# Performance work log

Measured on AMD Instinct MI355X. Metric: run time of the kernel, lower is better.

Reference implementation:

```python
import jax, jax.numpy as jnp
import numpy as np
from jax import lax

B = 64          # graphs per batch
N0 = 1024       # nodes per graph (equal-sized graphs -> static topk shapes)
DEG = 16        # avg degree
E = B * N0 * DEG
D_IN, D_H, D_OUT = 100, 128, 256
RATIO, EPS = 0.5, 1e-5


def _seg_sum(v, idx, n):
    return jax.ops.segment_sum(v, idx, num_segments=n)


def _gcn(x, src, dst, w_e, W, b, n):
    h = x @ W
    deg = 1.0 + _seg_sum(w_e, dst, n)          # +1 for self-loop
    dinv = lax.rsqrt(deg)
    norm = (dinv[src] * dinv[dst] * w_e)[:, None]
    return _seg_sum(h[src] * norm, dst, n) + h / deg[:, None] + b


def _graphnorm(x, w, bias, ms, nb, k):
    # PyG GraphNorm: per-graph mean/var with learnable mean_scale
    xg = x.reshape(nb, k, -1)
    mean = xg.mean(1, keepdims=True)
    sub = xg - ms * mean
    var = (sub * sub).mean(1, keepdims=True)
    return (w * sub * lax.rsqrt(var + EPS) + bias).reshape(nb * k, -1)


def _topk(x, src, dst, emask, p, nb, n_per):
    # TopKPooling (min_score=None): score = tanh(x.p/||p||), keep top ceil(r*n)
    k = int(np.ceil(RATIO * n_per))
    score = jnp.tanh((x @ p) / jnp.linalg.norm(p))
    vals, idx = lax.top_k(score.reshape(nb, n_per), k)            # [nb, k]
    perm = (idx + (jnp.arange(nb) * n_per)[:, None]).reshape(-1)
    x_new = x[perm] * vals.reshape(-1)[:, None]
    mapping = jnp.full((nb * n_per,), -1, jnp.int32).at[perm].set(
        jnp.arange(nb * k, dtype=jnp.int32))
    ns, nd = mapping[src], mapping[dst]
    valid = emask & (ns >= 0) & (nd >= 0)   # filter_adj as a persistent mask
    return x_new, jnp.where(valid, ns, 0), jnp.where(valid, nd, 0), valid, k


def _forward(x, edge_index, W1, b1, W2, b2, W3, b3,
             gn1_w, gn1_b, gn1_ms, gn2_w, gn2_b, gn2_ms,
             gn3_w, gn3_b, gn3_ms, p1, p2, p3):
    src, dst = edge_index[0], edge_index[1]
    emask = jnp.ones(src.shape, bool)
    Ws, bs = (W1, W2, W3), (b1, b2, b3)
    gw = (gn1_w, gn2_w, gn3_w)
    gb = (gn1_b, gn2_b, gn3_b)
    gm = (gn1_ms, gn2_ms, gn3_ms)
    ps = (p1, p2, p3)
    n_per = N0
    for i in range(3):
        n = B * n_per
        x = _gcn(x, src, dst, emask.astype(x.dtype), Ws[i], bs[i], n)
        x = _graphnorm(x, gw[i], gb[i], gm[i], B, n_per)
        x = jax.nn.relu(x)              # dropout: identity in eval mode
        x, src, dst, emask, n_per = _topk(x, src, dst, emask, ps[i], B, n_per)
    xg = x.reshape(B, n_per, D_OUT)
    # global mean/max pool then concat -> [B, 2*D_OUT]
    return jnp.concatenate([xg.mean(1), xg.max(1)], axis=1)


def setup_inputs():
    key = jax.random.key(0)
    ks = jax.random.split(key, 20)
    x = jax.random.normal(ks[0], (B * N0, D_IN), jnp.float32)
    # random edges within each graph, then offset by graph base index
    e = jax.random.randint(ks[1], (2, B, N0 * DEG), 0, N0, jnp.int32)
    edge_index = (e + (jnp.arange(B, dtype=jnp.int32) * N0)[None, :, None]).reshape(2, -1)
    batch = jnp.repeat(jnp.arange(B, dtype=jnp.int32), N0)
    inp = dict(x=x, edge_index=edge_index, batch=batch)
    dims = [(D_IN, D_H), (D_H, D_H), (D_H, D_OUT)]
    for i, (di, do) in enumerate(dims, 1):
        inp[f"W{i}"] = jax.random.normal(ks[1 + i], (di, do), jnp.float32) / np.sqrt(di)
        inp[f"b{i}"] = jnp.zeros((do,), jnp.float32)
        inp[f"gn{i}_w"] = jnp.ones((do,), jnp.float32)
        inp[f"gn{i}_b"] = jnp.zeros((do,), jnp.float32)
        inp[f"gn{i}_ms"] = jnp.ones((do,), jnp.float32)
        inp[f"p{i}"] = jax.random.normal(ks[10 + i], (do,), jnp.float32)
    return inp


def reference(x, edge_index, batch, W1, b1, W2, b2, W3, b3,
              gn1_w, gn1_b, gn1_ms, gn2_w, gn2_b, gn2_ms,
              gn3_w, gn3_b, gn3_ms, p1, p2, p3):
    del batch  # equal-sized graphs: grouping is encoded by constants B, N0
    return _forward(x, edge_index, W1, b1, W2, b2, W3, b3,
                    gn1_w, gn1_b, gn1_ms, gn2_w, gn2_b, gn2_ms,
                    gn3_w, gn3_b, gn3_ms, p1, p2, p3)
```

## Files before the change

### kernel.cpp

```cpp
#include <hip/hip_runtime.h>

#define GN_EPS 1e-5f

constexpr int NB   = 64;
constexpr int EPG  = 16384;
constexpr int ETOT = NB * EPG;
constexpr int NTOT = 64 * 1024;

__global__ void cmap_init_kernel(int* __restrict__ cmap) {
    int i = blockIdx.x * blockDim.x + threadIdx.x;
    if (i < NTOT) cmap[i] = i;
}

template <int NPG>
__global__ __launch_bounds__(1024) void csr_build_kernel(
        const int* __restrict__ ei, const int* __restrict__ cmap,
        int* __restrict__ cnt, int* __restrict__ offs, float* __restrict__ dinv,
        int2* __restrict__ csr_pack) {
    __shared__ int   lcnt[NPG];
    __shared__ float sdv[NPG];
    __shared__ int   wsum[16];
    constexpr int NW = NPG / 64;
    const int g = blockIdx.x;
    const int t = threadIdx.x;
    const int ebase = g * EPG;
    constexpr int EPT = EPG / 1024;

    for (int i = t; i < NPG; i += 1024) lcnt[i] = 0;
    __syncthreads();

    int ms_[EPT], md_[EPT];
#pragma unroll
    for (int i = 0; i < EPT; i++) {
        int e = ebase + t + i * 1024;
        int s = cmap[ei[e]];
        int d = cmap[ei[ETOT + e]];
        bool ok = (s >= 0) && (d >= 0);
        ms_[i] = ok ? s : -1;
        md_[i] = ok ? (d - g * NPG) : 0;
        if (ok) atomicAdd(&lcnt[d - g * NPG], 1);
    }
    __syncthreads();

    const int lane = t & 63;
    const int wid  = t >> 6;
    int orig = (t < NPG) ? lcnt[t] : 0;
    int v = orig;
#pragma unroll
    for (int d = 1; d < 64; d <<= 1) {
        int u = __shfl_up(v, d);
        if (lane >= d) v += u;
    }
    if (lane == 63) wsum[wid] = v;
    __syncthreads();
    if (wid == 0) {
        int wv = (lane < NW) ? wsum[lane] : 0;
#pragma unroll
        for (int d = 1; d < 16; d <<= 1) {
            int u = __shfl_up(wv, d);
            if (lane >= d) wv += u;
        }
        if (lane < NW) wsum[lane] = wv;
    }
    __syncthreads();
    if (t < NPG) {
        int incl = v + ((wid > 0) ? wsum[wid - 1] : 0);
        int excl = incl - orig;
        float dv = rsqrtf(1.0f + (float)orig);
        cnt[g * NPG + t]  = orig;
        offs[g * NPG + t] = ebase + excl;
        dinv[g * NPG + t] = dv;
        sdv[t] = dv;
        lcnt[t] = excl;
    }
    __syncthreads();

#pragma unroll
    for (int i = 0; i < EPT; i++) {
        int s = ms_[i];
        if (s >= 0) {
            int pos = atomicAdd(&lcnt[md_[i]], 1);
            csr_pack[ebase + pos] = make_int2(s, __float_as_int(sdv[s - g * NPG]));
        }
    }
}

template <int D4>
__global__ __launch_bounds__(256) void gather_kernel(
        const float* __restrict__ x, const int* __restrict__ cnt,
        const int* __restrict__ offs, const float* __restrict__ dinv,
        const int2* __restrict__ csr_pack, float* __restrict__ z, int n, int bpg) {
    constexpr int GRP = 8;
    constexpr int NPB = 256 / GRP;
    constexpr int CPL = 4;
    int bid   = blockIdx.x;
    int xcd   = bid & 7;
    int slot  = bid >> 3;
    int graph = xcd + 8 * (slot / bpg);
    int local = slot % bpg;
    int vb    = graph * bpg + local;

    int grp  = threadIdx.x / GRP;
    int lane = threadIdx.x % GRP;
    int v = vb * NPB + grp;
    if (v >= n) return;

    const float4* x4 = reinterpret_cast<const float4*>(x);
    int st = offs[v];
    int c  = cnt[v];
    float dv = dinv[v];

    int f4_[CPL];
    bool act[CPL];
#pragma unroll
    for (int i = 0; i < CPL; i++) {
        f4_[i] = lane + GRP * i;
        act[i] = f4_[i] < D4;
    }

    float4 acc[CPL];
#pragma unroll
    for (int i = 0; i < CPL; i++) {
        if (act[i]) {
            float4 xv = x4[(size_t)v * D4 + f4_[i]];
            acc[i] = {xv.x * dv, xv.y * dv, xv.z * dv, xv.w * dv};
        } else {
            acc[i] = {0.f, 0.f, 0.f, 0.f};
        }
    }

    const int nfull = c & ~3;
    int2 pk[4];
    if (nfull > 0) {
#pragma unroll
        for (int u = 0; u < 4; u++) pk[u] = csr_pack[st + u];
    }
    for (int j = 0; j < nfull; j += 4) {
        int2 cur0 = pk[0], cur1 = pk[1], cur2 = pk[2], cur3 = pk[3];
        if (j + 8 <= nfull) {
#pragma unroll
            for (int u = 0; u < 4; u++) pk[u] = csr_pack[st + j + 4 + u];
        }
        float d0 = __int_as_float(cur0.y), d1 = __int_as_float(cur1.y);
        float d2 = __int_as_float(cur2.y), d3 = __int_as_float(cur3.y);
        size_t r0 = (size_t)cur0.x * D4, r1 = (size_t)cur1.x * D4;
        size_t r2 = (size_t)cur2.x * D4, r3 = (size_t)cur3.x * D4;
#pragma unroll
        for (int i = 0; i < CPL; i++) {
            if (!act[i]) continue;
            float4 h0 = x4[r0 + f4_[i]];
            float4 h1 = x4[r1 + f4_[i]];
            float4 h2 = x4[r2 + f4_[i]];
            float4 h3 = x4[r3 + f4_[i]];
            acc[i].x += h0.x * d0 + h1.x * d1 + h2.x * d2 + h3.x * d3;
            acc[i].y += h0.y * d0 + h1.y * d1 + h2.y * d2 + h3.y * d3;
            acc[i].z += h0.z * d0 + h1.z * d1 + h2.z * d2 + h3.z * d3;
            acc[i].w += h0.w * d0 + h1.w * d1 + h2.w * d2 + h3.w * d3;
        }
    }
    for (int j = nfull; j < c; j++) {
        int2 p0 = csr_pack[st + j];
        float d0 = __int_as_float(p0.y);
        size_t r0 = (size_t)p0.x * D4;
#pragma unroll
        for (int i = 0; i < CPL; i++) {
            if (!act[i]) continue;
            float4 h0 = x4[r0 + f4_[i]];
            acc[i].x += h0.x * d0; acc[i].y += h0.y * d0;
            acc[i].z += h0.z * d0; acc[i].w += h0.w * d0;
        }
    }
#pragma unroll
    for (int i = 0; i < CPL; i++) {
        if (!act[i]) continue;
        float4 o = {acc[i].x * dv, acc[i].y * dv, acc[i].z * dv, acc[i].w * dv};
        reinterpret_cast<float4*>(z)[(size_t)v * D4 + f4_[i]] = o;
    }
}

__global__ __launch_bounds__(256) void gemm128_kernel(const float* __restrict__ A,
                                                      const float* __restrict__ W,
                                                      const float* __restrict__ Bias,
                                                      float* __restrict__ C,
                                                      float* __restrict__ sum1,
                                                      float* __restrict__ sum2,
                                                      int M, int N, int K, int nper) {
    __shared__ float As[16][132];
    __shared__ float Bs[16][132];
    __shared__ float red1[4][132];
    __shared__ float red2[4][132];
    const int bm = blockIdx.x * 128;
    const int bn = blockIdx.y * 128;
    const int tid = threadIdx.x;
    const int tx = tid & 15, ty = tid >> 4;

    const int arow = tid >> 1;
    const int ak   = (tid & 1) * 8;
    const int brow = tid >> 5;
    const int bc4  = (tid & 31) * 4;

    float acc[2][2][4][4] = {};

    for (int k0 = 0; k0 < K; k0 += 16) {
        {
            const float* ap = A + (size_t)(bm + arow) * K + k0 + ak;
            float4 a0 = {0,0,0,0}, a1 = {0,0,0,0};
            if (k0 + ak < K)     a0 = *reinterpret_cast<const float4*>(ap);
            if (k0 + ak + 4 < K) a1 = *reinterpret_cast<const float4*>(ap + 4);
            As[ak + 0][arow] = a0.x; As[ak + 1][arow] = a0.y;
            As[ak + 2][arow] = a0.z; As[ak + 3][arow] = a0.w;
            As[ak + 4][arow] = a1.x; As[ak + 5][arow] = a1.y;
            As[ak + 6][arow] = a1.z; As[ak + 7][arow] = a1.w;
        }
        {
            float4 b0 = {0,0,0,0}, b1 = {0,0,0,0};
            if (k0 + brow < K)
                b0 = *reinterpret_cast<const float4*>(W + (size_t)(k0 + brow) * N + bn + bc4);
            if (k0 + brow + 8 < K)
                b1 = *reinterpret_cast<const float4*>(W + (size_t)(k0 + brow + 8) * N + bn + bc4);
            *reinterpret_cast<float4*>(&Bs[brow][bc4])     = b0;
            *reinterpret_cast<float4*>(&Bs[brow + 8][bc4]) = b1;
        }
        __syncthreads();
#pragma unroll
        for (int k = 0; k < 16; k++) {
            float4 a0 = *reinterpret_cast<const float4*>(&As[k][ty * 4]);
            float4 a1 = *reinterpret_cast<const float4*>(&As[k][64 + ty * 4]);
            float4 b0 = *reinterpret_cast<const float4*>(&Bs[k][tx * 4]);
            float4 b1 = *reinterpret_cast<const float4*>(&Bs[k][64 + tx * 4]);
            const float av[2][4] = {{a0.x, a0.y, a0.z, a0.w}, {a1.x, a1.y, a1.z, a1.w}};
            const float bv[2][4] = {{b0.x, b0.y, b0.z, b0.w}, {b1.x, b1.y, b1.z, b1.w}};
#pragma unroll
            for (int qi = 0; qi < 2; qi++)
#pragma unroll
                for (int qj = 0; qj < 2; qj++)
#pragma unroll
                    for (int i = 0; i < 4; i++)
#pragma unroll
                        for (int j = 0; j < 4; j++)
                            acc[qi][qj][i][j] += av[qi][i] * bv[qj][j];
        }
        __syncthreads();
    }
    float4 bb[2];
    bb[0] = *reinterpret_cast<const float4*>(&Bias[bn + tx * 4]);
    bb[1] = *reinterpret_cast<const float4*>(&Bias[bn + 64 + tx * 4]);

    float s1l[2][4] = {}, s2l[2][4] = {};
#pragma unroll
    for (int qi = 0; qi < 2; qi++)
#pragma unroll
        for (int i = 0; i < 4; i++) {
            int row = bm + qi * 64 + ty * 4 + i;
#pragma unroll
            for (int qj = 0; qj < 2; qj++) {
                float o0 = acc[qi][qj][i][0] + bb[qj].x;
                float o1 = acc[qi][qj][i][1] + bb[qj].y;
                float o2 = acc[qi][qj][i][2] + bb[qj].z;
                float o3 = acc[qi][qj][i][3] + bb[qj].w;
                float4 o = {o0, o1, o2, o3};
                *reinterpret_cast<float4*>(&C[(size_t)row * N + bn + qj * 64 + tx * 4]) = o;
                s1l[qj][0] += o0; s2l[qj][0] += o0 * o0;
                s1l[qj][1] += o1; s2l[qj][1] += o1 * o1;
                s1l[qj][2] += o2; s2l[qj][2] += o2 * o2;
                s1l[qj][3] += o3; s2l[qj][3] += o3 * o3;
            }
        }
    const int wv = tid >> 6;
#pragma unroll
    for (int qj = 0; qj < 2; qj++)
#pragma unroll
        for (int j = 0; j < 4; j++) {
            float v1 = s1l[qj][j], v2 = s2l[qj][j];
            v1 += __shfl_xor(v1, 16); v1 += __shfl_xor(v1, 32);
            v2 += __shfl_xor(v2, 16); v2 += __shfl_xor(v2, 32);
            if ((tid & 48) == 0) {
                red1[wv][tx * 8 + qj * 4 + j] = v1;
                red2[wv][tx * 8 + qj * 4 + j] = v2;
            }
        }
    __syncthreads();
    if (tid < 16) {
        const int g   = bm / nper;
        const int nch = nper >> 7;
        const int ch  = (bm % nper) >> 7;
        size_t slotbase = (size_t)(g * nch + ch) * N + bn;
#pragma unroll
        for (int qj = 0; qj < 2; qj++)
#pragma unroll
            for (int j = 0; j < 4; j++) {
                int k = tid * 8 + qj * 4 + j;
                float v1 = red1[0][k] + red1[1][k] + red1[2][k] + red1[3][k];
                float v2 = red2[0][k] + red2[1][k] + red2[2][k] + red2[3][k];
                sum1[slotbase + qj * 64 + tid * 4 + j] = v1;
                sum2[slotbase + qj * 64 + tid * 4 + j] = v2;
            }
    }
}

__global__ void pnorm3_kernel(const float* __restrict__ p0, const float* __restrict__ p1,
                              const float* __restrict__ p2, int d0, int d1, int d2,
                              float* __restrict__ out) {
    __shared__ float red[256];
    const float* p = (blockIdx.x == 0) ? p0 : (blockIdx.x == 1) ? p1 : p2;
    int d          = (blockIdx.x == 0) ? d0 : (blockIdx.x == 1) ? d1 : d2;
    int t = threadIdx.x;
    float v = (t < d) ? p[t] : 0.0f;
    red[t] = v * v;
    __syncthreads();
    for (int s = 128; s; s >>= 1) {
        if (t < s) red[t] += red[t + s];
        __syncthreads();
    }
    if (t == 0) out[blockIdx.x] = 1.0f / sqrtf(red[0]);
}

template <int DO>
__global__ __launch_bounds__(256) void gn_apply_score_kernel(
        float* __restrict__ x, const float* __restrict__ sum1, const float* __restrict__ sum2,
        const float* __restrict__ ms, const float* __restrict__ w,
        const float* __restrict__ bias, const float* __restrict__ p,
        const float* __restrict__ pinv, float* __restrict__ score, int n_per, int nch) {
    constexpr int V = DO / 64;
    __shared__ float scm[DO];
    __shared__ float ssr[DO];
    int node = blockIdx.x * 4 + (threadIdx.x >> 6);
    int lane = threadIdx.x & 63;
    int g = node / n_per;
    float inv_n = 1.0f / (float)n_per;
    for (int f = threadIdx.x; f < DO; f += 256) {
        float s1 = 0.f, s2 = 0.f;
        for (int ch = 0; ch < nch; ch++) {
            s1 += sum1[(size_t)(g * nch + ch) * DO + f];
            s2 += sum2[(size_t)(g * nch + ch) * DO + f];
        }
        float mean = s1 * inv_n;
        float ex2  = s2 * inv_n;
        float m = ms[f];
        float var = ex2 - 2.f * m * mean * mean + m * m * mean * mean;
        scm[f] = m * mean;
        ssr[f] = w[f] * rsqrtf(var + GN_EPS);
    }
    __syncthreads();

    float*       xr = x + (size_t)node * DO + lane * V;
    const float* bb = bias + lane * V;
    const float* pp = p + lane * V;
    float dot = 0.f;
#pragma unroll
    for (int i = 0; i < V; i++) {
        int f = lane * V + i;
        float y = (xr[i] - scm[f]) * ssr[f] + bb[i];
        y = fmaxf(y, 0.0f);
        xr[i] = y;
        dot += y * pp[i];
    }
#pragma unroll
    for (int off = 32; off; off >>= 1) dot += __shfl_xor(dot, off);
    if (lane == 0) score[node] = tanhf(dot * pinv[0]);
}

template <int N, int K>
__global__ __launch_bounds__(1024) void topk_radix_kernel(
        const float* __restrict__ score, int* __restrict__ mapping,
        int* __restrict__ inv) {
    __shared__ int hist[256];
    __shared__ int sscan[N];
    __shared__ int sbyte, sneed;
    const int g = blockIdx.x;
    const int t = threadIdx.x;
    float sc = score[g * N + t];
    unsigned u = __float_as_uint(sc);
    unsigned key = (u & 0x80000000u) ? ~u : (u | 0x80000000u);

    unsigned prefix = 0;
    int need = K;
#pragma unroll
    for (int shift = 24; shift >= 0; shift -= 8) {
        if (t < 256) hist[t] = 0;
        __syncthreads();
        unsigned hm = (shift == 24) ? 0u : (0xFFFFFFFFu << (shift + 8));
        if ((key & hm) == (prefix & hm))
            atomicAdd(&hist[(key >> shift) & 255], 1);
        __syncthreads();
        if (t < 256) sscan[t] = hist[t];
        __syncthreads();
        for (int d = 1; d < 256; d <<= 1) {
            int x = (t < 256 && t + d < 256) ? sscan[t + d] : 0;
            __syncthreads();
            if (t < 256) sscan[t] += x;
            __syncthreads();
        }
        if (t < 256) {
            int ge  = sscan[t];
            int gt_ = (t + 1 < 256) ? sscan[t + 1] : 0;
            if (ge >= need && gt_ < need) { sbyte = t; sneed = need - gt_; }
        }
        __syncthreads();
        prefix |= ((unsigned)sbyte << shift);
        need = sneed;
        __syncthreads();
    }
    bool gt = key > prefix;
    bool eq = (key == prefix);
    sscan[t] = (gt ? (1 << 16) : 0) | (eq ? 1 : 0);
    __syncthreads();
    for (int d = 1; d < N; d <<= 1) {
        int x = (t >= d) ? sscan[t - d] : 0;
        __syncthreads();
        sscan[t] += x;
        __syncthreads();
    }
    int incl   = sscan[t];
    int gtrank = (incl >> 16) - (gt ? 1 : 0);
    int eqrank = (incl & 0xFFFF) - (eq ? 1 : 0);
    int cntGT  = K - need;
    bool sel = gt || (eq && (eqrank < need));
    int old_g = g * N + t;
    if (sel) {
        int slot = gt ? gtrank : (cntGT + eqrank);
        mapping[old_g] = g * K + slot;
        inv[g * K + slot] = old_g;
    } else {
        mapping[old_g] = -1;
    }
}

__global__ void permute_compose_kernel(const float* __restrict__ x, const int* __restrict__ inv,
                                       const float* __restrict__ score, float* __restrict__ xn,
                                       int total, int ldof4,
                                       int* __restrict__ cmap, const int* __restrict__ mapping) {
    int t = blockIdx.x * blockDim.x + threadIdx.x;
    if (t < total) {
        int node = t >> ldof4;
        int f4   = t & ((1 << ldof4) - 1);
        int dof4 = 1 << ldof4;
        int old = inv[node];
        float sc = score[old];
        float4 v = reinterpret_cast<const float4*>(x)[(size_t)old * dof4 + f4];
        float4 o = {v.x * sc, v.y * sc, v.z * sc, v.w * sc};
        reinterpret_cast<float4*>(xn)[t] = o;
    }
    if (t < NTOT) {
        int c = cmap[t];
        cmap[t] = (c >= 0) ? mapping[c] : -1;
    }
}

__global__ __launch_bounds__(1024) void pool_sel_kernel(const float* __restrict__ x,
                                                        const int* __restrict__ inv,
                                                        const float* __restrict__ score,
                                                        float* __restrict__ out) {
    __shared__ float ssum[1024];
    __shared__ float smax[1024];
    int g = blockIdx.x;
    int f = threadIdx.x & 255;
    int ch = threadIdx.x >> 8;
    float s = 0.f, mx = -INFINITY;
    for (int i = ch; i < 128; i += 4) {
        int old = inv[g * 128 + i];
        float sc = score[old];
        float v = x[(size_t)old * 256 + f] * sc;
        s += v;
        mx = fmaxf(mx, v);
    }
    ssum[threadIdx.x] = s;
    smax[threadIdx.x] = mx;
    __syncthreads();
    if (ch == 0) {
#pragma unroll
        for (int c = 1; c < 4; c++) {
            s  += ssum[f + c * 256];
            mx  = fmaxf(mx, smax[f + c * 256]);
        }
        out[g * 512 + f]       = s / 128.0f;
        out[g * 512 + 256 + f] = mx;
    }
}

static inline int cdiv_h(int a, int b) { return (a + b - 1) / b; }

extern "C" void kernel_launch(void* const* d_in, const int* in_sizes, int n_in,
                              void* d_out, int out_size, void* d_ws, size_t ws_size,
                              hipStream_t stream) {
    (void)in_sizes; (void)n_in; (void)out_size; (void)ws_size;

    const float* x_in = (const float*)d_in[0];
    const int*   ei   = (const int*)d_in[1];
    const float* Wm[3]  = {(const float*)d_in[3],  (const float*)d_in[9],  (const float*)d_in[15]};
    const float* bv[3]  = {(const float*)d_in[4],  (const float*)d_in[10], (const float*)d_in[16]};
    const float* gnw[3] = {(const float*)d_in[5],  (const float*)d_in[11], (const float*)d_in[17]};
    const float* gnb[3] = {(const float*)d_in[6],  (const float*)d_in[12], (const float*)d_in[18]};
    const float* gnm[3] = {(const float*)d_in[7],  (const float*)d_in[13], (const float*)d_in[19]};
    const float* pv[3]  = {(const float*)d_in[8],  (const float*)d_in[14], (const float*)d_in[20]};

    size_t off = 0;
    auto alloc = [&](size_t bytes) {
        void* p = (char*)d_ws + off;
        off += (bytes + 255) & ~(size_t)255;
        return p;
    };
    float* X1      = (float*)alloc((size_t)65536 * 128 * 4);
    float* Z       = (float*)alloc((size_t)65536 * 128 * 4);
    float* X2      = (float*)alloc((size_t)32768 * 128 * 4);
    int2*  csr_pack= (int2*)alloc((size_t)ETOT * 8);
    int*   cmap    = (int*)alloc(NTOT * 4);
    int*   cnt     = (int*)alloc(65536 * 4);
    int*   offs    = (int*)alloc(65536 * 4);
    float* dinv    = (float*)alloc(65536 * 4);
    float* score   = (float*)alloc(65536 * 4);
    int*   mapping = (int*)alloc(65536 * 4);
    int*   inv     = (int*)alloc(32768 * 4);
    float* sum1    = (float*)alloc(64 * 8 * 256 * 4);
    float* sum2    = (float*)alloc(64 * 8 * 256 * 4);
    float* pinv    = (float*)alloc(256);

    const int nper[4] = {1024, 512, 256, 128};
    const int din[3]  = {100, 128, 128};
    const int dof[3]  = {128, 128, 256};

    cmap_init_kernel<<<NTOT / 256, 256, 0, stream>>>(cmap);
    pnorm3_kernel<<<3, 256, 0, stream>>>(pv[0], pv[1], pv[2], dof[0], dof[1], dof[2], pinv);

    for (int L = 0; L < 3; L++) {
        const int n    = NB * nper[L];
        const int k    = nper[L + 1];
        const int nn   = NB * k;
        const int D    = dof[L];
        const int dof4 = D / 4;
        const int ldof4 = (dof4 == 32) ? 5 : 6;
        const int nch  = nper[L] / 128;
        const float* xin = (L == 0) ? x_in : X2;

        if (nper[L] == 1024)
            csr_build_kernel<1024><<<NB, 1024, 0, stream>>>(ei, cmap, cnt, offs, dinv, csr_pack);
        else if (nper[L] == 512)
            csr_build_kernel<512><<<NB, 1024, 0, stream>>>(ei, cmap, cnt, offs, dinv, csr_pack);
        else
            csr_build_kernel<256><<<NB, 1024, 0, stream>>>(ei, cmap, cnt, offs, dinv, csr_pack);

        {
            const int NPB = 32;
            const int bpg = nper[L] / NPB;
            if (L == 0)
                gather_kernel<25><<<n / NPB, 256, 0, stream>>>(xin, cnt, offs, dinv,
                                                               csr_pack, Z, n, bpg);
            else
                gather_kernel<32><<<n / NPB, 256, 0, stream>>>(xin, cnt, offs, dinv,
                                                               csr_pack, Z, n, bpg);
        }

        gemm128_kernel<<<dim3(n / 128, D / 128), 256, 0, stream>>>(Z, Wm[L], bv[L], X1,
                                                                   sum1, sum2,
                                                                   n, D, din[L], nper[L]);

        if (D == 128)
            gn_apply_score_kernel<128><<<n / 4, 256, 0, stream>>>(X1, sum1, sum2, gnm[L],
                                                                  gnw[L], gnb[L], pv[L],
                                                                  pinv + L, score, nper[L], nch);
        else
            gn_apply_score_kernel<256><<<n / 4, 256, 0, stream>>>(X1, sum1, sum2, gnm[L],
                                                                  gnw[L], gnb[L], pv[L],
                                                                  pinv + L, score, nper[L], nch);

        if (nper[L] == 1024)
            topk_radix_kernel<1024, 512><<<NB, 1024, 0, stream>>>(score, mapping, inv);
        else if (nper[L] == 512)
            topk_radix_kernel<512, 256><<<NB, 512, 0, stream>>>(score, mapping, inv);
        else
            topk_radix_kernel<256, 128><<<NB, 256, 0, stream>>>(score, mapping, inv);

        if (L < 2) {
            int total = nn * dof4;
            permute_compose_kernel<<<cdiv_h(total, 256), 256, 0, stream>>>(
                X1, inv, score, X2, total, ldof4, cmap, mapping);
        } else {
            pool_sel_kernel<<<NB, 1024, 0, stream>>>(X1, inv, score, (float*)d_out);
        }
    }
}
```

Before: 316.3 us.

## Stage layer-0 features in LDS per graph and fold cmap compose into CSR build

```diff
diff --git a/kernel.cpp b/kernel.cpp
--- a/kernel.cpp
+++ b/kernel.cpp
@@ -14,7 +14,8 @@
 
 template <int NPG>
 __global__ __launch_bounds__(1024) void csr_build_kernel(
-        const int* __restrict__ ei, const int* __restrict__ cmap,
+        const int* __restrict__ ei, int* __restrict__ cmap,
+        const int* __restrict__ mapping, int do_compose,
         int* __restrict__ cnt, int* __restrict__ offs, float* __restrict__ dinv,
         int2* __restrict__ csr_pack) {
     __shared__ int   lcnt[NPG];
@@ -26,6 +27,11 @@
     const int ebase = g * EPG;
     constexpr int EPT = EPG / 1024;
 
+    if (do_compose) {
+        int i = g * 1024 + t;
+        int c = cmap[i];
+        cmap[i] = (c >= 0) ? mapping[c] : -1;
+    }
     for (int i = t; i < NPG; i += 1024) lcnt[i] = 0;
     __syncthreads();
 
@@ -82,6 +88,75 @@
             int pos = atomicAdd(&lcnt[md_[i]], 1);
             csr_pack[ebase + pos] = make_int2(s, __float_as_int(sdv[s - g * NPG]));
         }
+    }
+}
+
+__global__ __launch_bounds__(1024) void gather_lds_kernel(
+        const float* __restrict__ x, const int* __restrict__ cnt,
+        const int* __restrict__ offs, const float* __restrict__ dinv,
+        const int2* __restrict__ csr_pack, float* __restrict__ z) {
+    __shared__ float4 slds[4096];
+    constexpr int D4 = 25;
+    const int g = blockIdx.x;
+    const int t = threadIdx.x;
+    const int v = g * 1024 + t;
+    const float4* x4 = reinterpret_cast<const float4*>(x);
+    float4* z4 = reinterpret_cast<float4*>(z);
+    const int st = offs[v];
+    const int c  = cnt[v];
+    const float dv = dinv[v];
+    const int sw = t & 3;
+
+    for (int c0 = 0; c0 < 24; c0 += 4) {
+        {
+            int node = t >> 2;
+#pragma unroll
+            for (int r = 0; r < 4; r++) {
+                int nd = node + r * 256;
+                int col = t & 3;
+                slds[nd * 4 + (col ^ (nd & 3))] = x4[(size_t)(g * 1024 + nd) * D4 + c0 + col];
+            }
+        }
+        __syncthreads();
+        float4 acc[4];
+#pragma unroll
+        for (int i = 0; i < 4; i++) {
+            float4 s = slds[t * 4 + (i ^ sw)];
+            acc[i] = {s.x * dv, s.y * dv, s.z * dv, s.w * dv};
+        }
+        for (int j = 0; j < c; j++) {
+            int2 p = csr_pack[st + j];
+            int ls = p.x - g * 1024;
+            float d = __int_as_float(p.y);
+            int lsw = ls & 3;
+#pragma unroll
+            for (int i = 0; i < 4; i++) {
+                float4 h = slds[ls * 4 + (i ^ lsw)];
+                acc[i].x += h.x * d; acc[i].y += h.y * d;
+                acc[i].z += h.z * d; acc[i].w += h.w * d;
+            }
+        }
+#pragma unroll
+        for (int i = 0; i < 4; i++) {
+            float4 o = {acc[i].x * dv, acc[i].y * dv, acc[i].z * dv, acc[i].w * dv};
+            z4[(size_t)v * D4 + c0 + i] = o;
+        }
+        __syncthreads();
+    }
+    slds[t] = x4[(size_t)v * D4 + 24];
+    __syncthreads();
+    {
+        float4 s = slds[t];
+        float4 acc = {s.x * dv, s.y * dv, s.z * dv, s.w * dv};
+        for (int j = 0; j < c; j++) {
+            int2 p = csr_pack[st + j];
+            int ls = p.x - g * 1024;
+            float d = __int_as_float(p.y);
+            float4 h = slds[ls];
+            acc.x += h.x * d; acc.y += h.y * d; acc.z += h.z * d; acc.w += h.w * d;
+        }
+        float4 o = {acc.x * dv, acc.y * dv, acc.z * dv, acc.w * dv};
+        z4[(size_t)v * D4 + 24] = o;
     }
 }
 
@@ -111,60 +186,40 @@
     float dv = dinv[v];
 
     int f4_[CPL];
-    bool act[CPL];
+#pragma unroll
+    for (int i = 0; i < CPL; i++) f4_[i] = lane + GRP * i;
+
+    float4 acc[CPL];
 #pragma unroll
     for (int i = 0; i < CPL; i++) {
-        f4_[i] = lane + GRP * i;
-        act[i] = f4_[i] < D4;
-    }
-
-    float4 acc[CPL];
-#pragma unroll
-    for (int i = 0; i < CPL; i++) {
-        if (act[i]) {
-            float4 xv = x4[(size_t)v * D4 + f4_[i]];
-            acc[i] = {xv.x * dv, xv.y * dv, xv.z * dv, xv.w * dv};
-        } else {
-            acc[i] = {0.f, 0.f, 0.f, 0.f};
-        }
-    }
-
-    const int nfull = c & ~3;
-    int2 pk[4];
-    if (nfull > 0) {
-#pragma unroll
-        for (int u = 0; u < 4; u++) pk[u] = csr_pack[st + u];
-    }
-    for (int j = 0; j < nfull; j += 4) {
-        int2 cur0 = pk[0], cur1 = pk[1], cur2 = pk[2], cur3 = pk[3];
-        if (j + 8 <= nfull) {
-#pragma unroll
-            for (int u = 0; u < 4; u++) pk[u] = csr_pack[st + j + 4 + u];
-        }
-        float d0 = __int_as_float(cur0.y), d1 = __int_as_float(cur1.y);
-        float d2 = __int_as_float(cur2.y), d3 = __int_as_float(cur3.y);
-        size_t r0 = (size_t)cur0.x * D4, r1 = (size_t)cur1.x * D4;
-        size_t r2 = (size_t)cur2.x * D4, r3 = (size_t)cur3.x * D4;
+        float4 xv = x4[(size_t)v * D4 + f4_[i]];
+        acc[i] = {xv.x * dv, xv.y * dv, xv.z * dv, xv.w * dv};
+    }
+
+    int j = 0;
+    for (; j + 2 <= c; j += 2) {
+        int2 p0 = csr_pack[st + j];
+        int2 p1 = csr_pack[st + j + 1];
+        float d0 = __int_as_float(p0.y);
+        float d1 = __int_as_float(p1.y);
+        size_t r0 = (size_t)p0.x * D4;
+        size_t r1 = (size_t)p1.x * D4;
 #pragma unroll
         for (int i = 0; i < CPL; i++) {
-            if (!act[i]) continue;
             float4 h0 = x4[r0 + f4_[i]];
             float4 h1 = x4[r1 + f4_[i]];
-            float4 h2 = x4[r2 + f4_[i]];
-            float4 h3 = x4[r3 + f4_[i]];
-            acc[i].x += h0.x * d0 + h1.x * d1 + h2.x * d2 + h3.x * d3;
-            acc[i].y += h0.y * d0 + h1.y * d1 + h2.y * d2 + h3.y * d3;
-            acc[i].z += h0.z * d0 + h1.z * d1 + h2.z * d2 + h3.z * d3;
-            acc[i].w += h0.w * d0 + h1.w * d1 + h2.w * d2 + h3.w * d3;
-        }
-    }
-    for (int j = nfull; j < c; j++) {
+            acc[i].x += h0.x * d0 + h1.x * d1;
+            acc[i].y += h0.y * d0 + h1.y * d1;
+            acc[i].z += h0.z * d0 + h1.z * d1;
+            acc[i].w += h0.w * d0 + h1.w * d1;
+        }
+    }
+    if (j < c) {
         int2 p0 = csr_pack[st + j];
         float d0 = __int_as_float(p0.y);
         size_t r0 = (size_t)p0.x * D4;
 #pragma unroll
         for (int i = 0; i < CPL; i++) {
-            if (!act[i]) continue;
             float4 h0 = x4[r0 + f4_[i]];
             acc[i].x += h0.x * d0; acc[i].y += h0.y * d0;
             acc[i].z += h0.z * d0; acc[i].w += h0.w * d0;
@@ -172,7 +227,6 @@
     }
 #pragma unroll
     for (int i = 0; i < CPL; i++) {
-        if (!act[i]) continue;
         float4 o = {acc[i].x * dv, acc[i].y * dv, acc[i].z * dv, acc[i].w * dv};
         reinterpret_cast<float4*>(z)[(size_t)v * D4 + f4_[i]] = o;
     }
@@ -426,25 +480,19 @@
     }
 }
 
-__global__ void permute_compose_kernel(const float* __restrict__ x, const int* __restrict__ inv,
-                                       const float* __restrict__ score, float* __restrict__ xn,
-                                       int total, int ldof4,
-                                       int* __restrict__ cmap, const int* __restrict__ mapping) {
+__global__ void permute_scale_kernel(const float* __restrict__ x, const int* __restrict__ inv,
+                                     const float* __restrict__ score, float* __restrict__ xn,
+                                     int total, int ldof4) {
     int t = blockIdx.x * blockDim.x + threadIdx.x;
-    if (t < total) {
-        int node = t >> ldof4;
-        int f4   = t & ((1 << ldof4) - 1);
-        int dof4 = 1 << ldof4;
-        int old = inv[node];
-        float sc = score[old];
-        float4 v = reinterpret_cast<const float4*>(x)[(size_t)old * dof4 + f4];
-        float4 o = {v.x * sc, v.y * sc, v.z * sc, v.w * sc};
-        reinterpret_cast<float4*>(xn)[t] = o;
-    }
-    if (t < NTOT) {
-        int c = cmap[t];
-        cmap[t] = (c >= 0) ? mapping[c] : -1;
-    }
+    if (t >= total) return;
+    int node = t >> ldof4;
+    int f4   = t & ((1 << ldof4) - 1);
+    int dof4 = 1 << ldof4;
+    int old = inv[node];
+    float sc = score[old];
+    float4 v = reinterpret_cast<const float4*>(x)[(size_t)old * dof4 + f4];
+    float4 o = {v.x * sc, v.y * sc, v.z * sc, v.w * sc};
+    reinterpret_cast<float4*>(xn)[t] = o;
 }
 
 __global__ __launch_bounds__(1024) void pool_sel_kernel(const float* __restrict__ x,
@@ -533,21 +581,22 @@
         const float* xin = (L == 0) ? x_in : X2;
 
         if (nper[L] == 1024)
-            csr_build_kernel<1024><<<NB, 1024, 0, stream>>>(ei, cmap, cnt, offs, dinv, csr_pack);
+            csr_build_kernel<1024><<<NB, 1024, 0, stream>>>(ei, cmap, mapping, 0,
+                                                            cnt, offs, dinv, csr_pack);
         else if (nper[L] == 512)
-            csr_build_kernel<512><<<NB, 1024, 0, stream>>>(ei, cmap, cnt, offs, dinv, csr_pack);
+            csr_build_kernel<512><<<NB, 1024, 0, stream>>>(ei, cmap, mapping, 1,
+                                                           cnt, offs, dinv, csr_pack);
         else
-            csr_build_kernel<256><<<NB, 1024, 0, stream>>>(ei, cmap, cnt, offs, dinv, csr_pack);
-
-        {
+            csr_build_kernel<256><<<NB, 1024, 0, stream>>>(ei, cmap, mapping, 1,
+                                                           cnt, offs, dinv, csr_pack);
+
+        if (L == 0) {
+            gather_lds_kernel<<<NB, 1024, 0, stream>>>(xin, cnt, offs, dinv, csr_pack, Z);
+        } else {
             const int NPB = 32;
             const int bpg = nper[L] / NPB;
-            if (L == 0)
-                gather_kernel<25><<<n / NPB, 256, 0, stream>>>(xin, cnt, offs, dinv,
-                                                               csr_pack, Z, n, bpg);
-            else
-                gather_kernel<32><<<n / NPB, 256, 0, stream>>>(xin, cnt, offs, dinv,
-                                                               csr_pack, Z, n, bpg);
+            gather_kernel<32><<<n / NPB, 256, 0, stream>>>(xin, cnt, offs, dinv,
+                                                           csr_pack, Z, n, bpg);
         }
 
         gemm128_kernel<<<dim3(n / 128, D / 128), 256, 0, stream>>>(Z, Wm[L], bv[L], X1,
@@ -572,8 +621,8 @@
 
         if (L < 2) {
             int total = nn * dof4;
-            permute_compose_kernel<<<cdiv_h(total, 256), 256, 0, stream>>>(
-                X1, inv, score, X2, total, ldof4, cmap, mapping);
+            permute_scale_kernel<<<cdiv_h(total, 256), 256, 0, stream>>>(
+                X1, inv, score, X2, total, ldof4);
         } else {
             pool_sel_kernel<<<NB, 1024, 0, stream>>>(X1, inv, score, (float*)d_out);
         }
```

Measured after the change: 393.4 us. +24.4%, slower.
